# Performance work log

Measured on AMD Instinct MI355X. Metric: run time of the kernel, lower is better.

Reference implementation:

```python
import jax, jax.numpy as jnp
import numpy as np

N = 100000   # nodes
E = 1600000  # edges
G = 1000     # graphs
S = 32       # state_dim
H = 128      # hidden_dim_message / hidden_dim_output
F = 1        # num_features (edge coulomb)
ROUNDS = 5
NEG_SLOPE = 0.01
LN_EPS = 1e-5


def _ln(x, g, b):
    m = jnp.mean(x, axis=-1, keepdims=True)
    v = jnp.var(x, axis=-1, keepdims=True)
    return (x - m) / jnp.sqrt(v + LN_EPS) * g + b


def _lrelu(x):
    return jnp.where(x >= 0, x, NEG_SLOPE * x)


def _kaiming(k, shape):
    # torch kaiming_normal_(mode='fan_out', nonlinearity='leaky_relu'); W stored [in,out]
    gain = np.sqrt(2.0 / (1.0 + NEG_SLOPE ** 2))
    std = gain / np.sqrt(shape[1])
    return jax.random.normal(k, shape, dtype=jnp.float32) * std


def setup_inputs() -> dict:
    key = jax.random.key(0)
    ks = jax.random.split(key, 10)
    return {
        'node_from': jax.random.randint(ks[0], (E,), 0, N),
        'node_to': jax.random.randint(ks[1], (E,), 0, N),
        'edge_coulomb': jax.random.normal(ks[2], (E, F), dtype=jnp.float32),
        'node_graph_index': jax.random.randint(ks[3], (N,), 0, G),
        'num_nodes': N,
        'num_graphs': G,
        # message_net params
        'W1': _kaiming(ks[4], (S + F, H)), 'b1': jnp.zeros((H,), jnp.float32),
        'g1': jnp.ones((H,), jnp.float32), 'be1': jnp.zeros((H,), jnp.float32),
        'W2': _kaiming(ks[5], (H, S)), 'b2': jnp.zeros((S,), jnp.float32),
        'g2': jnp.ones((S,), jnp.float32), 'be2': jnp.zeros((S,), jnp.float32),
        # output_net params
        'Wo1': _kaiming(ks[6], (S, H)), 'bo1': jnp.zeros((H,), jnp.float32),
        'go': jnp.ones((H,), jnp.float32), 'beo': jnp.zeros((H,), jnp.float32),
        'Wo2': _kaiming(ks[7], (H, 2)), 'bo2': jnp.zeros((2,), jnp.float32),
    }


def reference(node_from, node_to, edge_coulomb, node_graph_index, num_nodes, num_graphs,
              W1, b1, g1, be1, W2, b2, g2, be2, Wo1, bo1, go, beo, Wo2, bo2):
    state = jnp.zeros((num_nodes, S), dtype=edge_coulomb.dtype)
    for _ in range(ROUNDS):
        inp = jnp.concatenate([state[node_from], edge_coulomb], axis=1)  # [E, S+F]
        h = _lrelu(_ln(inp @ W1 + b1, g1, be1))                           # [E, H]
        msg = _lrelu(_ln(h @ W2 + b2, g2, be2))                           # [E, S]
        state = state + jax.ops.segment_sum(msg, node_to, num_segments=num_nodes)
    graph_state = jax.ops.segment_sum(state, node_graph_index, num_segments=num_graphs)  # [G, S]
    h = _lrelu(_ln(graph_state @ Wo1 + bo1, go, beo))
    ev = h @ Wo2 + bo2                                                    # [G, 2]
    mu = ev[:, :1]
    var = jax.nn.softplus(ev[:, 1:])
    return jnp.concatenate([mu, var], axis=1)
```

## Files before the change

kernel.cpp:

```cpp
#include <hip/hip_runtime.h>
#include <hip/hip_bf16.h>

#define NN 100000
#define NE 1600000
#define NG 1000
#define SS 32
#define HH 128
#define ROUNDS 5

constexpr float NEG = 0.01f;
constexpr float EPS = 1e-5f;

constexpr long al4(long x)  { return (x + 3) & ~3L; }
constexpr long al16(long x) { return (x + 15) & ~15L; }

constexpr long OFF_STATE = 0;
constexpr long OFF_GS    = OFF_STATE + (long)NN * SS;
constexpr long OFF_W1T   = OFF_GS + (long)NG * SS;
constexpr long OFF_B1    = OFF_W1T + HH * 33;
constexpr long OFF_G1    = OFF_B1 + HH;
constexpr long OFF_BE1   = OFF_G1 + HH;
constexpr long OFF_W2    = OFF_BE1 + HH;
constexpr long OFF_B2    = OFF_W2 + HH * SS;
constexpr long OFF_G2    = OFF_B2 + SS;
constexpr long OFF_BE2   = OFF_G2 + SS;
constexpr long OFF_WO1   = OFF_BE2 + SS;
constexpr long OFF_BO1   = OFF_WO1 + SS * HH;
constexpr long OFF_GO    = OFF_BO1 + HH;
constexpr long OFF_BEO   = OFF_GO + HH;
constexpr long OFF_WO2   = OFF_BEO + HH;
constexpr long OFF_BO2   = OFF_WO2 + HH * 2;
constexpr long OFF_W1L   = al4(OFF_BO2 + 2);
constexpr long OFF_WSC   = OFF_W1L + HH;
constexpr long OFF_W1B   = al4(OFF_WSC + 2);
constexpr long OFF_W2F   = OFF_W1B + 2048;
constexpr long OFF_WPK   = OFF_W2F + 2048;
constexpr long OFF_Z0P   = OFF_WPK + 192;
constexpr long W_END     = OFF_Z0P + 68;
constexpr long OFF_DELTA = al4(W_END);
constexpr long F_Z      = al4(W_END);
constexpr long F_START  = al4(F_Z + (long)NN * 68);
constexpr long F_CURSOR = F_START + NN + 4;
constexpr long F_SSTART = F_CURSOR + NN;
constexpr long F_SCUR   = F_SSTART + NN + 4;
constexpr long F_BSUM   = F_SCUR + NN;
constexpr long F_GDEG   = F_BSUM + 512;
constexpr long F_GSTART = F_GDEG + NG;
constexpr long F_GCUR   = F_GSTART + NG + 4;
constexpr long F_GLIST  = F_GCUR + NG;
constexpr long F_EPK    = al16(F_GLIST + NN);
constexpr long F_SP     = F_EPK + (long)NE * 2;
constexpr long F_MSG    = al16(F_SP + NE);
constexpr long F_RC     = F_MSG;
constexpr long WS_TOTAL = F_MSG + (long)NE * 16;
constexpr long WS_FALLBACK = OFF_DELTA + (long)NN * SS;
constexpr int  NBLK_N  = (NN + 255) / 256;
constexpr int  CHSHIFT_E = 19;
constexpr int  NCH_E     = (NE + (1 << CHSHIFT_E) - 1) >> CHSHIFT_E;
constexpr int  CHSHIFT_P = 20;
constexpr int  NCH_P     = (NE + (1 << CHSHIFT_P) - 1) >> CHSHIFT_P;

typedef float f32x4 __attribute__((ext_vector_type(4)));
typedef unsigned int u32x4 __attribute__((ext_vector_type(4)));
typedef short s16x8 __attribute__((ext_vector_type(8)));

__device__ __forceinline__ s16x8 as_s16x8(u32x4 u) {
    union { u32x4 a; s16x8 b; } c; c.a = u; return c.b;
}
__device__ __forceinline__ float bf2f(unsigned short u) {
    union { unsigned int i; float f; } v;
    v.i = ((unsigned int)u) << 16;
    return v.f;
}
__device__ __forceinline__ float lo_bf(unsigned int p) {
    union { unsigned int i; float f; } v; v.i = p << 16; return v.f;
}
__device__ __forceinline__ float hi_bf(unsigned int p) {
    union { unsigned int i; float f; } v; v.i = p & 0xFFFF0000u; return v.f;
}
__device__ __forceinline__ unsigned short f2bf(float f) {
    union { float f; unsigned int u; } x; x.f = f;
    return (unsigned short)((x.u + 0x7FFFu + ((x.u >> 16) & 1u)) >> 16);
}
__device__ __forceinline__ unsigned int pack_bf2(float a, float b) {
    return (unsigned int)f2bf(a) | ((unsigned int)f2bf(b) << 16);
}
#if defined(__has_builtin)
#if __has_builtin(__builtin_amdgcn_cvt_pk_bf16_f32)
#define HAVE_CVT_PK_BF16 1
#endif
#endif
__device__ __forceinline__ unsigned int cvt2bf(float a, float b) {
#ifdef HAVE_CVT_PK_BF16
    auto r = __builtin_amdgcn_cvt_pk_bf16_f32(a, b);
    unsigned int u; __builtin_memcpy(&u, &r, 4); return u;
#else
    return pack_bf2(a, b);
#endif
}
template <int CTRL>
__device__ __forceinline__ float ror_add(float x) {
    int v = __builtin_amdgcn_update_dpp(0, __float_as_int(x), CTRL, 0xF, 0xF, true);
    return x + __int_as_float(v);
}
__device__ __forceinline__ float row_reduce16(float x) {
    x = ror_add<0x121>(x);
    x = ror_add<0x122>(x);
    x = ror_add<0x124>(x);
    x = ror_add<0x128>(x);
    return x;
}
__device__ __forceinline__ int is_bf16(const void* g1raw) {
    return (((const unsigned int*)g1raw)[0] & 0xFFFFu) != 0u;
}
__device__ __forceinline__ float ldf(const void* p, long idx, int bf) {
    return bf ? bf2f(((const unsigned short*)p)[idx]) : ((const float*)p)[idx];
}

__global__ void prep_kernel(
    const void* __restrict__ W1,  const void* __restrict__ b1,
    const void* __restrict__ g1,  const void* __restrict__ be1,
    const void* __restrict__ W2,  const void* __restrict__ b2,
    const void* __restrict__ g2,  const void* __restrict__ be2,
    const void* __restrict__ Wo1, const void* __restrict__ bo1,
    const void* __restrict__ go,  const void* __restrict__ beo,
    const void* __restrict__ Wo2, const void* __restrict__ bo2,
    float* __restrict__ ws)
{
    const int bf = is_bf16(g1);
    long idx = (long)blockIdx.x * blockDim.x + threadIdx.x;
    if (idx < (long)NN * SS) { ws[OFF_STATE + idx] = 0.f; ws[OFF_DELTA + idx] = 0.f; }
    if (idx < (long)NG * SS) ws[OFF_GS + idx] = 0.f;
    if (idx < NN) { ((int*)(ws + F_CURSOR))[idx] = 0; ((int*)(ws + F_SCUR))[idx] = 0; }
    if (idx < NG) ((int*)(ws + F_GDEG))[idx] = 0;
    if (idx < 33 * HH) {
        int i = (int)(idx / HH), k = (int)(idx % HH);
        ws[OFF_W1T + (long)k * 33 + i] = ldf(W1, idx, bf);
    }
    if (idx < HH) {
        ws[OFF_B1  + idx] = ldf(b1,  idx, bf);
        ws[OFF_G1  + idx] = ldf(g1,  idx, bf);
        ws[OFF_BE1 + idx] = ldf(be1, idx, bf);
        ws[OFF_BO1 + idx] = ldf(bo1, idx, bf);
        ws[OFF_GO  + idx] = ldf(go,  idx, bf);
        ws[OFF_BEO + idx] = ldf(beo, idx, bf);
        ws[OFF_W1L + idx] = ldf(W1, (long)32 * HH + idx, bf);
    }
    if (idx == 0) {
        float sw = 0.f, sq = 0.f;
        float sb = 0.f, qb = 0.f, db = 0.f;
        for (int i = 0; i < HH; i++) {
            float w = ldf(W1, (long)32 * HH + i, bf);
            float x = ldf(b1, i, bf);
            sw += w; sq = fmaf(w, w, sq);
            sb += x; qb = fmaf(x, x, qb); db = fmaf(x, w, db);
        }
        ws[OFF_WSC] = sw; ws[OFF_WSC + 1] = sq;
        float* z0s = ws + OFF_Z0P + 64;
        z0s[0] = sb; z0s[1] = qb; z0s[2] = db; z0s[3] = 0.f;
    }
    if (idx < 64) {
        ((unsigned int*)(ws + OFF_Z0P))[idx] =
            cvt2bf(ldf(b1, 2 * idx, bf), ldf(b1, 2 * idx + 1, bf));
    }
    if (idx < HH * SS) ws[OFF_W2 + idx] = ldf(W2, idx, bf);
    if (idx < SS) {
        ws[OFF_B2  + idx] = ldf(b2,  idx, bf);
        ws[OFF_G2  + idx] = ldf(g2,  idx, bf);
        ws[OFF_BE2 + idx] = ldf(be2, idx, bf);
    }
    if (idx < SS * HH) ws[OFF_WO1 + idx] = ldf(Wo1, idx, bf);
    if (idx < HH * 2)  ws[OFF_WO2 + idx] = ldf(Wo2, idx, bf);
    if (idx < 2)       ws[OFF_BO2 + idx] = ldf(bo2, idx, bf);
    if (idx < 2048) {
        int w = (int)idx;
        int qq = w & 3, L = (w >> 2) & 63, t = (int)(w >> 8);
        int k0 = (L >> 4) * 8 + 2 * qq;
        int n  = t * 16 + (L & 15);
        ((unsigned int*)(ws + OFF_W1B))[w] =
            pack_bf2(ldf(W1, (long)k0 * HH + n, bf), ldf(W1, (long)(k0 + 1) * HH + n, bf));
    }
    if (idx < 2048) {
        int w = (int)idx;
        int qq = w & 3, L = (w >> 2) & 63, t2 = (w >> 8) & 1, ks = (int)(w >> 9);
        int k0 = ks * 32 + (L >> 4) * 8 + 2 * qq;
        int n  = t2 * 16 + (L & 15);
        float v0 = ldf(W2, (long)k0 * SS + n, bf);
        float v1 = ldf(W2, (long)(k0 + 1) * SS + n, bf);
        ((unsigned int*)(ws + OFF_W2F))[w] = pack_bf2(v0, v1);
    }
    if (idx < 192) {
        int w = (int)idx;
        int grp = w / 12, rem = w % 12, slot = rem >> 2, q = rem & 3;
        int ks = grp >> 2, quad = grp & 3;
        int n = ks * 32 + quad * 8 + 2 * q;
        float v0, v1;
        if (slot == 0)      { v0 = ldf(W1, (long)32 * HH + n, bf); v1 = ldf(W1, (long)32 * HH + n + 1, bf); }
        else if (slot == 1) { v0 = ldf(g1, n, bf);  v1 = ldf(g1, n + 1, bf); }
        else                { v0 = ldf(be1, n, bf); v1 = ldf(be1, n + 1, bf); }
        ((unsigned int*)(ws + OFF_WPK))[w] = pack_bf2(v0, v1);
    }
}

__global__ void fillseq_kernel(const int* __restrict__ nfrom, const int* __restrict__ nto,
                               float* ws) {
    int e = blockIdx.x * 256 + threadIdx.x;
    if (e < NE) {
        int u = nfrom[e];
        int v = nto[e];
        int drank = atomicAdd(&((int*)(ws + F_CURSOR))[v], 1);
        int srank = atomicAdd(&((int*)(ws + F_SCUR))[u], 1);
        uint2 o; o.x = (unsigned int)drank; o.y = (unsigned int)srank;
        *(uint2*)((unsigned int*)(ws + F_RC) + (long)e * 2) = o;
    }
}

__global__ void scan1_kernel(float* ws, long degOff, long startOff) {
    __shared__ int sh[256];
    int* deg   = (int*)(ws + degOff);
    int* start = (int*)(ws + startOff);
    int* bsum  = (int*)(ws + F_BSUM);
    int i = blockIdx.x * 256 + threadIdx.x;
    int x = (i < NN) ? deg[i] : 0;
    sh[threadIdx.x] = x;
    __syncthreads();
    for (int off = 1; off < 256; off <<= 1) {
        int t = (threadIdx.x >= off) ? sh[threadIdx.x - off] : 0;
        __syncthreads();
        sh[threadIdx.x] += t;
        __syncthreads();
    }
    int incl = sh[threadIdx.x];
    if (i < NN) start[i] = incl - x;
    if (threadIdx.x == 255) bsum[blockIdx.x] = incl;
}

__global__ void scan2p_kernel(float* ws) {
    __shared__ int sh[512];
    int* bsum = (int*)(ws + F_BSUM);
    int t = threadIdx.x;
    int x = (t < NBLK_N) ? bsum[t] : 0;
    sh[t] = x;
    __syncthreads();
    for (int off = 1; off < 512; off <<= 1) {
        int v = (t >= off) ? sh[t - off] : 0;
        __syncthreads();
        sh[t] += v;
        __syncthreads();
    }
    if (t < NBLK_N) bsum[t] = sh[t] - x;
}

__global__ void scan3_kernel(float* ws, long startOff) {
    int* start  = (int*)(ws + startOff);
    int* bsum   = (int*)(ws + F_BSUM);
    int i = blockIdx.x * 256 + threadIdx.x;
    if (i < NN) {
        start[i] += bsum[i >> 8];
        if (i == 0) start[NN] = NE;
    }
}

__global__ void epkc_kernel(const int* __restrict__ nfrom, const void* __restrict__ ec,
                            const void* __restrict__ g1raw, float* ws, int chunk) {
    int e = blockIdx.x * 256 + threadIdx.x;
    if (e < NE) {
        uint2 rc = *(const uint2*)((const unsigned int*)(ws + F_RC) + (long)e * 2);
        int u = nfrom[e];
        int spos = ((const int*)(ws + F_SSTART))[u] + (int)rc.y;
        if ((spos >> CHSHIFT_E) == chunk) {
            union { float f; unsigned int i; } c; c.f = ldf(ec, e, is_bf16(g1raw));
            uint2 o; o.x = (unsigned int)u; o.y = c.i;
            *(uint2*)((unsigned int*)(ws + F_EPK) + (long)spos * 2) = o;
        }
    }
}

__global__ void spc_kernel(const int* __restrict__ nfrom, const int* __restrict__ nto,
                           float* ws, int chunk) {
    int e = blockIdx.x * 256 + threadIdx.x;
    if (e < NE) {
        uint2 rc = *(const uint2*)((const unsigned int*)(ws + F_RC) + (long)e * 2);
        int dpos = ((const int*)(ws + F_START))[nto[e]] + (int)rc.x;
        if ((dpos >> CHSHIFT_P) == chunk) {
            int spos = ((const int*)(ws + F_SSTART))[nfrom[e]] + (int)rc.y;
            ((int*)(ws + F_SP))[dpos] = spos;
        }
    }
}

__global__ void ghist_kernel(const int* __restrict__ gidx, float* ws) {
    int i = blockIdx.x * 256 + threadIdx.x;
    if (i < NN) atomicAdd(&((int*)(ws + F_GDEG))[gidx[i]], 1);
}

__global__ void gscan_kernel(float* ws) {
    __shared__ int sh[1024];
    int* deg   = (int*)(ws + F_GDEG);
    int* start = (int*)(ws + F_GSTART);
    int* cur   = (int*)(ws + F_GCUR);
    int t = threadIdx.x;
    int x = (t < NG) ? deg[t] : 0;
    sh[t] = x;
    __syncthreads();
    for (int off = 1; off < 1024; off <<= 1) {
        int v = (t >= off) ? sh[t - off] : 0;
        __syncthreads();
        sh[t] += v;
        __syncthreads();
    }
    if (t < NG) { start[t] = sh[t] - x; cur[t] = sh[t] - x; }
    if (t == 0) start[NG] = NN;
}

__global__ void gfill_kernel(const int* __restrict__ gidx, float* ws) {
    int i = blockIdx.x * 256 + threadIdx.x;
    if (i < NN) {
        int pos = atomicAdd(&((int*)(ws + F_GCUR))[gidx[i]], 1);
        ((int*)(ws + F_GLIST))[pos] = i;
    }
}

__launch_bounds__(256)
__global__ void node_kernel(float* __restrict__ ws, const u32x4* __restrict__ mb, int do_z)
{
    __shared__ unsigned short zl[4][16 * 136];
    __shared__ float stl[64 * 33];
    const long nbase = (long)blockIdx.x * 64;

    {
        int t = threadIdx.x;
        int vl = t >> 2, sub = t & 3;
        long v = nbase + vl;
        if (v < NN) {
            const int* start = (const int*)(ws + F_START);
            const int* SPp   = (const int*)(ws + F_SP);
            int s0 = start[v], s1 = start[v + 1];
            float* st = ws + OFF_STATE + v * SS + sub * 8;
            float a0 = st[0], a1 = st[1], a2 = st[2], a3 = st[3];
            float a4 = st[4], a5 = st[5], a6 = st[6], a7 = st[7];
            int p = s0;
            for (; p + 7 < s1; p += 8) {
                int q0 = SPp[p],     q1 = SPp[p + 1], q2 = SPp[p + 2], q3 = SPp[p + 3];
                int q4 = SPp[p + 4], q5 = SPp[p + 5], q6 = SPp[p + 6], q7 = SPp[p + 7];
                u32x4 m0 = mb[(long)q0 * 4 + sub];
                u32x4 m1 = mb[(long)q1 * 4 + sub];
                u32x4 m2 = mb[(long)q2 * 4 + sub];
                u32x4 m3 = mb[(long)q3 * 4 + sub];
                u32x4 m4 = mb[(long)q4 * 4 + sub];
                u32x4 m5 = mb[(long)q5 * 4 + sub];
                u32x4 m6 = mb[(long)q6 * 4 + sub];
                u32x4 m7 = mb[(long)q7 * 4 + sub];
                a0 += lo_bf(m0[0]); a1 += hi_bf(m0[0]);
                a2 += lo_bf(m0[1]); a3 += hi_bf(m0[1]);
                a4 += lo_bf(m0[2]); a5 += hi_bf(m0[2]);
                a6 += lo_bf(m0[3]); a7 += hi_bf(m0[3]);
                a0 += lo_bf(m1[0]); a1 += hi_bf(m1[0]);
                a2 += lo_bf(m1[1]); a3 += hi_bf(m1[1]);
                a4 += lo_bf(m1[2]); a5 += hi_bf(m1[2]);
                a6 += lo_bf(m1[3]); a7 += hi_bf(m1[3]);
                a0 += lo_bf(m2[0]); a1 += hi_bf(m2[0]);
                a2 += lo_bf(m2[1]); a3 += hi_bf(m2[1]);
                a4 += lo_bf(m2[2]); a5 += hi_bf(m2[2]);
                a6 += lo_bf(m2[3]); a7 += hi_bf(m2[3]);
                a0 += lo_bf(m3[0]); a1 += hi_bf(m3[0]);
                a2 += lo_bf(m3[1]); a3 += hi_bf(m3[1]);
                a4 += lo_bf(m3[2]); a5 += hi_bf(m3[2]);
                a6 += lo_bf(m3[3]); a7 += hi_bf(m3[3]);
                a0 += lo_bf(m4[0]); a1 += hi_bf(m4[0]);
                a2 += lo_bf(m4[1]); a3 += hi_bf(m4[1]);
                a4 += lo_bf(m4[2]); a5 += hi_bf(m4[2]);
                a6 += lo_bf(m4[3]); a7 += hi_bf(m4[3]);
                a0 += lo_bf(m5[0]); a1 += hi_bf(m5[0]);
                a2 += lo_bf(m5[1]); a3 += hi_bf(m5[1]);
                a4 += lo_bf(m5[2]); a5 += hi_bf(m5[2]);
                a6 += lo_bf(m5[3]); a7 += hi_bf(m5[3]);
                a0 += lo_bf(m6[0]); a1 += hi_bf(m6[0]);
                a2 += lo_bf(m6[1]); a3 += hi_bf(m6[1]);
                a4 += lo_bf(m6[2]); a5 += hi_bf(m6[2]);
                a6 += lo_bf(m6[3]); a7 += hi_bf(m6[3]);
                a0 += lo_bf(m7[0]); a1 += hi_bf(m7[0]);
                a2 += lo_bf(m7[1]); a3 += hi_bf(m7[1]);
                a4 += lo_bf(m7[2]); a5 += hi_bf(m7[2]);
                a6 += lo_bf(m7[3]); a7 += hi_bf(m7[3]);
            }
            for (; p + 3 < s1; p += 4) {
                int q0 = SPp[p], q1 = SPp[p + 1], q2 = SPp[p + 2], q3 = SPp[p + 3];
                u32x4 m0 = mb[(long)q0 * 4 + sub];
                u32x4 m1 = mb[(long)q1 * 4 + sub];
                u32x4 m2 = mb[(long)q2 * 4 + sub];
                u32x4 m3 = mb[(long)q3 * 4 + sub];
                a0 += lo_bf(m0[0]); a1 += hi_bf(m0[0]);
                a2 += lo_bf(m0[1]); a3 += hi_bf(m0[1]);
                a4 += lo_bf(m0[2]); a5 += hi_bf(m0[2]);
                a6 += lo_bf(m0[3]); a7 += hi_bf(m0[3]);
                a0 += lo_bf(m1[0]); a1 += hi_bf(m1[0]);
                a2 += lo_bf(m1[1]); a3 += hi_bf(m1[1]);
                a4 += lo_bf(m1[2]); a5 += hi_bf(m1[2]);
                a6 += lo_bf(m1[3]); a7 += hi_bf(m1[3]);
                a0 += lo_bf(m2[0]); a1 += hi_bf(m2[0]);
                a2 += lo_bf(m2[1]); a3 += hi_bf(m2[1]);
                a4 += lo_bf(m2[2]); a5 += hi_bf(m2[2]);
                a6 += lo_bf(m2[3]); a7 += hi_bf(m2[3]);
                a0 += lo_bf(m3[0]); a1 += hi_bf(m3[0]);
                a2 += lo_bf(m3[1]); a3 += hi_bf(m3[1]);
                a4 += lo_bf(m3[2]); a5 += hi_bf(m3[2]);
                a6 += lo_bf(m3[3]); a7 += hi_bf(m3[3]);
            }
            for (; p < s1; ++p) {
                int spv = SPp[p];
                u32x4 m = mb[(long)spv * 4 + sub];
                a0 += lo_bf(m[0]); a1 += hi_bf(m[0]);
                a2 += lo_bf(m[1]); a3 += hi_bf(m[1]);
                a4 += lo_bf(m[2]); a5 += hi_bf(m[2]);
                a6 += lo_bf(m[3]); a7 += hi_bf(m[3]);
            }
            st[0] = a0; st[1] = a1; st[2] = a2; st[3] = a3;
            st[4] = a4; st[5] = a5; st[6] = a6; st[7] = a7;
            float* sl = stl + vl * 33 + sub * 8;
            sl[0] = a0; sl[1] = a1; sl[2] = a2; sl[3] = a3;
            sl[4] = a4; sl[5] = a5; sl[6] = a6; sl[7] = a7;
        }
    }
    if (!do_z) return;
    __syncthreads();

    const int wv = threadIdx.x >> 6, lane = threadIdx.x & 63;
    const int col = lane & 15, quad = lane >> 4;
    const long vbase = nbase + wv * 16;
    if (vbase >= NN) return;

    const float* sl = stl + (wv * 16 + col) * 33 + quad * 8;
    float st[8];
#pragma unroll
    for (int j = 0; j < 8; j++) st[j] = sl[j];

    u32x4 au;
    au[0] = cvt2bf(st[0], st[1]);
    au[1] = cvt2bf(st[2], st[3]);
    au[2] = cvt2bf(st[4], st[5]);
    au[3] = cvt2bf(st[6], st[7]);
    s16x8 af = as_s16x8(au);

    const u32x4* W1B = (const u32x4*)(ws + OFF_W1B);
    const float* B1 = ws + OFF_B1;
    f32x4 acc[8];
#pragma unroll
    for (int t = 0; t < 8; t++) {
        float bb = B1[t * 16 + col];
        acc[t][0] = bb; acc[t][1] = bb; acc[t][2] = bb; acc[t][3] = bb;
        acc[t] = __builtin_amdgcn_mfma_f32_16x16x32_bf16(af, as_s16x8(W1B[t * 64 + lane]), acc[t], 0, 0, 0);
    }

    float s[4] = {0.f, 0.f, 0.f, 0.f}, q[4] = {0.f, 0.f, 0.f, 0.f}, d[4] = {0.f, 0.f, 0.f, 0.f};
    const float* W1L = ws + OFF_W1L;
#pragma unroll
    for (int t = 0; t < 8; t++) {
        float wl = W1L[t * 16 + col];
#pragma unroll
        for (int r = 0; r < 4; r++) {
            float z = acc[t][r];
            s[r] += z; q[r] = fmaf(z, z, q[r]); d[r] = fmaf(z, wl, d[r]);
        }
    }
#pragma unroll
    for (int r = 0; r < 4; r++) {
        float sr = row_reduce16(s[r]);
        float qr = row_reduce16(q[r]);
        float dr = row_reduce16(d[r]);
        if (col == 0) {
            f32x4 o; o[0] = sr; o[1] = qr; o[2] = dr; o[3] = 0.f;
            *(f32x4*)(ws + F_Z + (vbase + quad * 4 + r) * 68 + 64) = o;
        }
    }

    unsigned short* zw_ = zl[wv];
#pragma unroll
    for (int t = 0; t < 8; t++) {
        unsigned int p01 = cvt2bf(acc[t][0], acc[t][1]);
        unsigned int p23 = cvt2bf(acc[t][2], acc[t][3]);
        unsigned short* b = zw_ + quad * (4 * 136) + t * 16 + col;
        b[0]       = (unsigned short)p01;
        b[136]     = (unsigned short)(p01 >> 16);
        b[2 * 136] = (unsigned short)p23;
        b[3 * 136] = (unsigned short)(p23 >> 16);
    }
    unsigned int* zg = (unsigned int*)(ws + F_Z);
#pragma unroll
    for (int it = 0; it < 4; it++) {
        int byte = it * 1024 + lane * 16;
        int node = byte >> 8;
        int ko   = (byte & 255) >> 2;
        u32x4 val = *(const u32x4*)(zw_ + node * 136 + ((byte & 255) >> 1));
        *(u32x4*)(zg + (vbase + node) * 68L + ko) = val;
    }
}

template <int R0>
__launch_bounds__(256)
__global__ void edge_src_kernel(const float* __restrict__ ws, uint2* __restrict__ msgout)
{
    const int lane = threadIdx.x & 63, wv = threadIdx.x >> 6;
    const int col = lane & 15, quad = lane >> 4;

    const u32x4* W2Fp = (const u32x4*)(ws + OFF_W2F);
    u32x4 w2f[8];
#pragma unroll
    for (int i = 0; i < 8; i++) w2f[i] = W2Fp[i * 64 + lane];
    u32x4 wlp[4], gp[4], bep[4];
    const u32x4* WPKp = (const u32x4*)(ws + OFF_WPK);
#pragma unroll
    for (int ks = 0; ks < 4; ks++) {
        const u32x4* W = WPKp + (ks * 4 + quad) * 3;
        wlp[ks] = W[0]; gp[ks] = W[1]; bep[ks] = W[2];
    }
    f32x4 g2h[2], be2h[2], b2h[2];
#pragma unroll
    for (int t2 = 0; t2 < 2; t2++) {
        g2h[t2]  = *(const f32x4*)(ws + OFF_G2  + t2 * 16 + quad * 4);
        be2h[t2] = *(const f32x4*)(ws + OFF_BE2 + t2 * 16 + quad * 4);
        b2h[t2]  = *(const f32x4*)(ws + OFF_B2  + t2 * 16 + quad * 4);
    }
    const float sw1 = ws[OFF_WSC], sqw1 = ws[OFF_WSC + 1];

    f32x4 zst0;
    u32x4 zw0[4];
    if (R0) {
        zst0 = *(const f32x4*)(ws + OFF_Z0P + 64);
#pragma unroll
        for (int ks = 0; ks < 4; ks++)
            zw0[ks] = *(const u32x4*)((const unsigned int*)(ws + OFF_Z0P) + ks * 16 + quad * 4);
    }

    const uint2* EPKp = (const uint2*)((const unsigned int*)(ws + F_EPK));
    const unsigned int* Zp = (const unsigned int*)(ws + F_Z);
    const long tbase = ((long)blockIdx.x * 4 + wv) * 4;

    uint2 epk[4];
#pragma unroll
    for (int k = 0; k < 4; k++)
        epk[k] = EPKp[(tbase + k) * 16 + col];
    f32x4 zst[4];
    u32x4 zwc[4];
    if (!R0) {
#pragma unroll
        for (int k = 0; k < 4; k++)
            zst[k] = *(const f32x4*)(ws + F_Z + (long)(int)epk[k].x * 68 + 64);
        const unsigned int* zrow0 = Zp + (long)(int)epk[0].x * 68;
#pragma unroll
        for (int ks = 0; ks < 4; ks++)
            zwc[ks] = *(const u32x4*)(zrow0 + ks * 16 + quad * 4);
    }

#pragma unroll
    for (int k = 0; k < 4; k++) {
        const int epos = (int)((tbase + k) * 16) + col;
        union { unsigned int i; float f; } cc; cc.i = epk[k].y;
        const float ecv = cc.f;

        u32x4 zwn[4];
        if (!R0 && k < 3) {
            const unsigned int* zrown = Zp + (long)(int)epk[k + 1].x * 68;
#pragma unroll
            for (int ks = 0; ks < 4; ks++)
                zwn[ks] = *(const u32x4*)(zrown + ks * 16 + quad * 4);
        }

        f32x4 zs = R0 ? zst0 : zst[k];
        float sumh = fmaf(ecv, sw1, zs[0]);
        float sqh  = fmaf(ecv, fmaf(ecv, sqw1, 2.f * zs[2]), zs[1]);
        float mean = sumh * (1.f / HH);
        float var  = fmaxf(sqh * (1.f / HH) - mean * mean, 0.f);
        float inv  = rsqrtf(var + EPS);
        const float alpha = inv, beta = -mean * inv;

        f32x4 acc2[2];
        acc2[0] = b2h[0]; acc2[1] = b2h[1];

#pragma unroll
        for (int ks = 0; ks < 4; ks++) {
            u32x4 zwv = R0 ? zw0[ks] : zwc[ks];
            u32x4 hu;
#pragma unroll
            for (int w = 0; w < 4; w++) {
                float z0 = lo_bf(zwv[w]), z1 = hi_bf(zwv[w]);
                float h0 = fmaf(ecv, lo_bf(wlp[ks][w]), z0);
                float h1 = fmaf(ecv, hi_bf(wlp[ks][w]), z1);
                h0 = fmaf(h0, alpha, beta);
                h1 = fmaf(h1, alpha, beta);
                h0 = fmaf(h0, lo_bf(gp[ks][w]), lo_bf(bep[ks][w]));
                h1 = fmaf(h1, hi_bf(gp[ks][w]), hi_bf(bep[ks][w]));
                h0 = fmaxf(h0, NEG * h0);
                h1 = fmaxf(h1, NEG * h1);
                hu[w] = cvt2bf(h0, h1);
            }
            s16x8 hf = as_s16x8(hu);
            acc2[0] = __builtin_amdgcn_mfma_f32_16x16x32_bf16(as_s16x8(w2f[ks * 2 + 0]), hf, acc2[0], 0, 0, 0);
            acc2[1] = __builtin_amdgcn_mfma_f32_16x16x32_bf16(as_s16x8(w2f[ks * 2 + 1]), hf, acc2[1], 0, 0, 0);
        }

        float s2 = 0.f, q2 = 0.f;
#pragma unroll
        for (int t2 = 0; t2 < 2; t2++)
#pragma unroll
            for (int r = 0; r < 4; r++) { float vv = acc2[t2][r]; s2 += vv; q2 = fmaf(vv, vv, q2); }
        s2 += __shfl_xor(s2, 16); q2 += __shfl_xor(q2, 16);
        s2 += __shfl_xor(s2, 32); q2 += __shfl_xor(q2, 32);
        float mean2 = s2 * (1.f / SS);
        float var2  = fmaxf(q2 * (1.f / SS) - mean2 * mean2, 0.f);
        float inv2  = rsqrtf(var2 + EPS);
        const float a2 = inv2, b2c = -mean2 * inv2;

        uint2* dst = msgout + (long)epos * 8;
#pragma unroll
        for (int t2 = 0; t2 < 2; t2++) {
            float m0 = fmaf(fmaf(acc2[t2][0], a2, b2c), g2h[t2][0], be2h[t2][0]);
            float m1 = fmaf(fmaf(acc2[t2][1], a2, b2c), g2h[t2][1], be2h[t2][1]);
            float m2 = fmaf(fmaf(acc2[t2][2], a2, b2c), g2h[t2][2], be2h[t2][2]);
            float m3 = fmaf(fmaf(acc2[t2][3], a2, b2c), g2h[t2][3], be2h[t2][3]);
            m0 = fmaxf(m0, NEG * m0); m1 = fmaxf(m1, NEG * m1);
            m2 = fmaxf(m2, NEG * m2); m3 = fmaxf(m3, NEG * m3);
            uint2 o; o.x = cvt2bf(m0, m1); o.y = cvt2bf(m2, m3);
            dst[t2 * 4 + quad] = o;
        }

        if (!R0 && k < 3) {
#pragma unroll
            for (int ks = 0; ks < 4; ks++) zwc[ks] = zwn[ks];
        }
    }
}

__launch_bounds__(256)
__global__ void graph_gather_kernel(float* __restrict__ ws)
{
    int t = blockIdx.x * 256 + threadIdx.x;
    int g = t >> 5;
    if (g >= NG) return;
    int j = t & 31;
    const int* start = (const int*)(ws + F_GSTART);
    const int* list  = (const int*)(ws + F_GLIST);
    int s0 = start[g], s1 = start[g + 1];
    float acc = 0.f;
    for (int p = s0; p < s1; ++p)
        acc += ws[OFF_STATE + (long)list[p] * SS + j];
    ws[OFF_GS + (long)g * SS + j] = acc;
}

__launch_bounds__(256)
__global__ void edge_atomic_kernel(const int* __restrict__ nfrom, const int* __restrict__ nto,
                                   const void* __restrict__ ec, const void* __restrict__ g1raw,
                                   const float* __restrict__ cws, float* delta)
{
    int e = blockIdx.x * 256 + threadIdx.x;
    if (e >= NE) return;
    const float* state = cws + OFF_STATE;
    const float* W1T = cws + OFF_W1T;
    const float* B1  = cws + OFF_B1;
    const float* G1  = cws + OFF_G1;
    const float* BE1 = cws + OFF_BE1;
    const float* W2  = cws + OFF_W2;
    const float* B2  = cws + OFF_B2;
    const float* G2  = cws + OFF_G2;
    const float* BE2 = cws + OFF_BE2;
    int u = nfrom[e];
    float inp[33];
    const float4* srow = (const float4*)(state + (long)u * SS);
#pragma unroll
    for (int i = 0; i < 8; i++) {
        float4 v = srow[i];
        inp[i * 4 + 0] = v.x; inp[i * 4 + 1] = v.y;
        inp[i * 4 + 2] = v.z; inp[i * 4 + 3] = v.w;
    }
    inp[32] = ldf(ec, e, is_bf16(g1raw));
    float sum = 0.f, sq = 0.f;
    for (int k = 0; k < HH; k++) {
        const float* wr = W1T + k * 33;
        float a = B1[k];
#pragma unroll
        for (int i = 0; i < 33; i++) a = fmaf(inp[i], wr[i], a);
        sum += a; sq = fmaf(a, a, sq);
    }
    float mean = sum * (1.f / HH);
    float var  = sq * (1.f / HH) - mean * mean;
    float inv  = rsqrtf(var + EPS);
    float msg[SS];
#pragma unroll
    for (int j = 0; j < SS; j++) msg[j] = B2[j];
    for (int k = 0; k < HH; k++) {
        const float* wr = W1T + k * 33;
        float a = B1[k];
#pragma unroll
        for (int i = 0; i < 33; i++) a = fmaf(inp[i], wr[i], a);
        float hk = fmaf((a - mean) * inv, G1[k], BE1[k]);
        hk = hk >= 0.f ? hk : NEG * hk;
        const float* w2r = W2 + k * SS;
#pragma unroll
        for (int j = 0; j < SS; j++) msg[j] = fmaf(hk, w2r[j], msg[j]);
    }
    float s2 = 0.f, q2 = 0.f;
#pragma unroll
    for (int j = 0; j < SS; j++) { s2 += msg[j]; q2 = fmaf(msg[j], msg[j], q2); }
    float m2 = s2 * (1.f / SS);
    float v2 = q2 * (1.f / SS) - m2 * m2;
    float i2 = rsqrtf(v2 + EPS);
    int v = nto[e];
    float* drow = delta + (long)v * SS;
#pragma unroll
    for (int j = 0; j < SS; j++) {
        float mj = fmaf((msg[j] - m2) * i2, G2[j], BE2[j]);
        mj = mj >= 0.f ? mj : NEG * mj;
        atomicAdd(drow + j, mj);
    }
}

__global__ void update_kernel(float* ws)
{
    long idx = (long)blockIdx.x * blockDim.x + threadIdx.x;
    if (idx < (long)NN * SS) {
        ws[OFF_STATE + idx] += ws[OFF_DELTA + idx];
        ws[OFF_DELTA + idx] = 0.f;
    }
}

__global__ void graph_kernel(const int* __restrict__ gidx, float* ws)
{
    long idx = (long)blockIdx.x * blockDim.x + threadIdx.x;
    if (idx < (long)NN * SS) {
        int i = (int)(idx >> 5);
        int j = (int)(idx & 31);
        atomicAdd(&ws[OFF_GS + (long)gidx[i] * SS + j], ws[OFF_STATE + idx]);
    }
}

__global__ void readout_kernel(const float* __restrict__ ws, const void* __restrict__ g1raw,
                               void* __restrict__ out)
{
    int g = blockIdx.x;
    int j = threadIdx.x;
    __shared__ float row[SS];
    __shared__ float buf[HH];
    __shared__ float p0[HH];
    __shared__ float p1[HH];

    const float* gs  = ws + OFF_GS;
    const float* Wo1 = ws + OFF_WO1;
    if (j < SS) row[j] = gs[(long)g * SS + j];
    __syncthreads();

    float a = ws[OFF_BO1 + j];
#pragma unroll
    for (int i = 0; i < SS; i++) a = fmaf(row[i], Wo1[i * HH + j], a);
    buf[j] = a;
    __syncthreads();

    float sum = 0.f, sq = 0.f;
    for (int i = 0; i < HH; i++) { float x = buf[i]; sum += x; sq = fmaf(x, x, sq); }
    float mean = sum * (1.f / HH);
    float var  = sq * (1.f / HH) - mean * mean;
    float inv  = rsqrtf(var + EPS);
    float h = fmaf((a - mean) * inv, ws[OFF_GO + j], ws[OFF_BEO + j]);
    h = h >= 0.f ? h : NEG * h;

    p0[j] = h * ws[OFF_WO2 + j * 2 + 0];
    p1[j] = h * ws[OFF_WO2 + j * 2 + 1];
    __syncthreads();

    if (j == 0) {
        float e0 = ws[OFF_BO2 + 0], e1 = ws[OFF_BO2 + 1];
        for (int i = 0; i < HH; i++) { e0 += p0[i]; e1 += p1[i]; }
        float sp = (e1 > 20.f) ? e1 : log1pf(expf(e1));
        if (is_bf16(g1raw)) {
            __hip_bfloat16* o = (__hip_bfloat16*)out;
            o[g * 2 + 0] = __float2bfloat16(e0);
            o[g * 2 + 1] = __float2bfloat16(sp);
        } else {
            float* o = (float*)out;
            o[g * 2 + 0] = e0;
            o[g * 2 + 1] = sp;
        }
    }
}

extern "C" void kernel_launch(void* const* d_in, const int* in_sizes, int n_in,
                              void* d_out, int out_size, void* d_ws, size_t ws_size,
                              hipStream_t stream)
{
    const int* nfrom = (const int*)d_in[0];
    const int* nto   = (const int*)d_in[1];
    const void* ec   = d_in[2];
    const int* gidx  = (const int*)d_in[3];
    const void* W1  = d_in[6];
    const void* b1  = d_in[7];
    const void* g1  = d_in[8];
    const void* be1 = d_in[9];
    const void* W2  = d_in[10];
    const void* b2  = d_in[11];
    const void* g2  = d_in[12];
    const void* be2 = d_in[13];
    const void* Wo1 = d_in[14];
    const void* bo1 = d_in[15];
    const void* go  = d_in[16];
    const void* beo = d_in[17];
    const void* Wo2 = d_in[18];
    const void* bo2 = d_in[19];

    float* ws = (float*)d_ws;
    if (ws_size < (size_t)WS_FALLBACK * sizeof(float)) return;
    const bool gather = ws_size >= (size_t)WS_TOTAL * sizeof(float);

    const int nsBlocks = (int)(((long)NN * SS + 255) / 256);
    const int eBlocks  = (NE + 255) / 256;
    const int efBlocks = NE / 256;
    const int ndBlocks = (NN + 63) / 64;
    const int nBlocks1 = (NN + 255) / 256;

    prep_kernel<<<nsBlocks, 256, 0, stream>>>(W1, b1, g1, be1, W2, b2, g2, be2,
                                              Wo1, bo1, go, beo, Wo2, bo2, ws);
    if (gather) {
        uint2* msgp = (uint2*)(ws + F_MSG);
        const u32x4* mbp = (const u32x4*)(ws + F_MSG);
        fillseq_kernel<<<eBlocks, 256, 0, stream>>>(nfrom, nto, ws);
        scan1_kernel<<<NBLK_N, 256, 0, stream>>>(ws, F_CURSOR, F_START);
        scan2p_kernel<<<1, 512, 0, stream>>>(ws);
        scan3_kernel<<<NBLK_N, 256, 0, stream>>>(ws, F_START);
        scan1_kernel<<<NBLK_N, 256, 0, stream>>>(ws, F_SCUR, F_SSTART);
        scan2p_kernel<<<1, 512, 0, stream>>>(ws);
        scan3_kernel<<<NBLK_N, 256, 0, stream>>>(ws, F_SSTART);
        for (int c = 0; c < NCH_E; c++)
            epkc_kernel<<<eBlocks, 256, 0, stream>>>(nfrom, ec, g1, ws, c);
        for (int c = 0; c < NCH_P; c++)
            spc_kernel<<<eBlocks, 256, 0, stream>>>(nfrom, nto, ws, c);
        ghist_kernel<<<nBlocks1, 256, 0, stream>>>(gidx, ws);
        gscan_kernel<<<1, 1024, 0, stream>>>(ws);
        gfill_kernel<<<nBlocks1, 256, 0, stream>>>(gidx, ws);
        for (int r = 0; r < ROUNDS; r++) {
            if (r == 0) edge_src_kernel<1><<<efBlocks, 256, 0, stream>>>(ws, msgp);
            else        edge_src_kernel<0><<<efBlocks, 256, 0, stream>>>(ws, msgp);
            node_kernel<<<ndBlocks, 256, 0, stream>>>(ws, mbp, (r < ROUNDS - 1) ? 1 : 0);
        }
        graph_gather_kernel<<<(NG * 32 + 255) / 256, 256, 0, stream>>>(ws);
    } else {
        for (int r = 0; r < ROUNDS; r++) {
            edge_atomic_kernel<<<eBlocks, 256, 0, stream>>>(nfrom, nto, ec, g1, ws, ws + OFF_DELTA);
            update_kernel<<<nsBlocks, 256, 0, stream>>>(ws);
        }
        graph_kernel<<<nsBlocks, 256, 0, stream>>>(gidx, ws);
    }
    readout_kernel<<<NG, HH, 0, stream>>>(ws, g1, (void*)d_out);
}
```

Measured before the change: 1.062 ms.

## Merge CSR conversion passes, pad Z rows, double edges per wave, skip unused zeroing

Fuses the chunked epkc and spc conversion loops into one chunked conv kernel that computes both source and destination positions per edge, cutting redundant passes over the edge arrays. Pads the per-node Z rows from 68 to 80 floats and aligns them to 16, so gathered row reads are better aligned. The edge kernel now processes two groups of 4 tiles per wave, halving the grid. The delta buffer is only zeroed on the fallback path, and LDS state stores are skipped when Z is not needed. Padding Z costs more workspace, and the wider per-wave loop reduces the number of waves available to hide gather latency.

```diff
diff --git a/kernel.cpp b/kernel.cpp
--- a/kernel.cpp
+++ b/kernel.cpp
@@ -13,6 +13,8 @@
 
 constexpr long al4(long x)  { return (x + 3) & ~3L; }
 constexpr long al16(long x) { return (x + 15) & ~15L; }
+
+constexpr int ZSTR = 80;
 
 constexpr long OFF_STATE = 0;
 constexpr long OFF_GS    = OFF_STATE + (long)NN * SS;
@@ -38,8 +40,8 @@
 constexpr long OFF_Z0P   = OFF_WPK + 192;
 constexpr long W_END     = OFF_Z0P + 68;
 constexpr long OFF_DELTA = al4(W_END);
-constexpr long F_Z      = al4(W_END);
-constexpr long F_START  = al4(F_Z + (long)NN * 68);
+constexpr long F_Z      = al16(W_END);
+constexpr long F_START  = al4(F_Z + (long)NN * ZSTR);
 constexpr long F_CURSOR = F_START + NN + 4;
 constexpr long F_SSTART = F_CURSOR + NN;
 constexpr long F_SCUR   = F_SSTART + NN + 4;
@@ -55,10 +57,8 @@
 constexpr long WS_TOTAL = F_MSG + (long)NE * 16;
 constexpr long WS_FALLBACK = OFF_DELTA + (long)NN * SS;
 constexpr int  NBLK_N  = (NN + 255) / 256;
-constexpr int  CHSHIFT_E = 19;
-constexpr int  NCH_E     = (NE + (1 << CHSHIFT_E) - 1) >> CHSHIFT_E;
-constexpr int  CHSHIFT_P = 20;
-constexpr int  NCH_P     = (NE + (1 << CHSHIFT_P) - 1) >> CHSHIFT_P;
+constexpr int  CHSHIFT_C = 19;
+constexpr int  NCH_C     = (NE + (1 << CHSHIFT_C) - 1) >> CHSHIFT_C;
 
 typedef float f32x4 __attribute__((ext_vector_type(4)));
 typedef unsigned int u32x4 __attribute__((ext_vector_type(4)));
@@ -125,11 +125,14 @@
     const void* __restrict__ Wo1, const void* __restrict__ bo1,
     const void* __restrict__ go,  const void* __restrict__ beo,
     const void* __restrict__ Wo2, const void* __restrict__ bo2,
-    float* __restrict__ ws)
+    float* __restrict__ ws, int zeroDelta)
 {
     const int bf = is_bf16(g1);
     long idx = (long)blockIdx.x * blockDim.x + threadIdx.x;
-    if (idx < (long)NN * SS) { ws[OFF_STATE + idx] = 0.f; ws[OFF_DELTA + idx] = 0.f; }
+    if (idx < (long)NN * SS) {
+        ws[OFF_STATE + idx] = 0.f;
+        if (zeroDelta) ws[OFF_DELTA + idx] = 0.f;
+    }
     if (idx < (long)NG * SS) ws[OFF_GS + idx] = 0.f;
     if (idx < NN) { ((int*)(ws + F_CURSOR))[idx] = 0; ((int*)(ws + F_SCUR))[idx] = 0; }
     if (idx < NG) ((int*)(ws + F_GDEG))[idx] = 0;
@@ -261,29 +264,22 @@
     }
 }
 
-__global__ void epkc_kernel(const int* __restrict__ nfrom, const void* __restrict__ ec,
-                            const void* __restrict__ g1raw, float* ws, int chunk) {
+__global__ void conv_kernel(const int* __restrict__ nfrom, const int* __restrict__ nto,
+                            const void* __restrict__ ec, const void* __restrict__ g1raw,
+                            float* ws, int chunk) {
     int e = blockIdx.x * 256 + threadIdx.x;
     if (e < NE) {
         uint2 rc = *(const uint2*)((const unsigned int*)(ws + F_RC) + (long)e * 2);
         int u = nfrom[e];
+        int v = nto[e];
         int spos = ((const int*)(ws + F_SSTART))[u] + (int)rc.y;
-        if ((spos >> CHSHIFT_E) == chunk) {
+        int dpos = ((const int*)(ws + F_START))[v] + (int)rc.x;
+        if ((spos >> CHSHIFT_C) == chunk) {
             union { float f; unsigned int i; } c; c.f = ldf(ec, e, is_bf16(g1raw));
             uint2 o; o.x = (unsigned int)u; o.y = c.i;
             *(uint2*)((unsigned int*)(ws + F_EPK) + (long)spos * 2) = o;
         }
-    }
-}
-
-__global__ void spc_kernel(const int* __restrict__ nfrom, const int* __restrict__ nto,
-                           float* ws, int chunk) {
-    int e = blockIdx.x * 256 + threadIdx.x;
-    if (e < NE) {
-        uint2 rc = *(const uint2*)((const unsigned int*)(ws + F_RC) + (long)e * 2);
-        int dpos = ((const int*)(ws + F_START))[nto[e]] + (int)rc.x;
-        if ((dpos >> CHSHIFT_P) == chunk) {
-            int spos = ((const int*)(ws + F_SSTART))[nfrom[e]] + (int)rc.y;
+        if ((dpos >> CHSHIFT_C) == chunk) {
             ((int*)(ws + F_SP))[dpos] = spos;
         }
     }
@@ -417,9 +413,11 @@
             }
             st[0] = a0; st[1] = a1; st[2] = a2; st[3] = a3;
             st[4] = a4; st[5] = a5; st[6] = a6; st[7] = a7;
-            float* sl = stl + vl * 33 + sub * 8;
-            sl[0] = a0; sl[1] = a1; sl[2] = a2; sl[3] = a3;
-            sl[4] = a4; sl[5] = a5; sl[6] = a6; sl[7] = a7;
+            if (do_z) {
+                float* sl = stl + vl * 33 + sub * 8;
+                sl[0] = a0; sl[1] = a1; sl[2] = a2; sl[3] = a3;
+                sl[4] = a4; sl[5] = a5; sl[6] = a6; sl[7] = a7;
+            }
         }
     }
     if (!do_z) return;
@@ -470,7 +468,7 @@
         float dr = row_reduce16(d[r]);
         if (col == 0) {
             f32x4 o; o[0] = sr; o[1] = qr; o[2] = dr; o[3] = 0.f;
-            *(f32x4*)(ws + F_Z + (vbase + quad * 4 + r) * 68 + 64) = o;
+            *(f32x4*)(ws + F_Z + (vbase + quad * 4 + r) * (long)ZSTR + 64) = o;
         }
     }
 
@@ -492,7 +490,7 @@
         int node = byte >> 8;
         int ko   = (byte & 255) >> 2;
         u32x4 val = *(const u32x4*)(zw_ + node * 136 + ((byte & 255) >> 1));
-        *(u32x4*)(zg + (vbase + node) * 68L + ko) = val;
+        *(u32x4*)(zg + (vbase + node) * (long)ZSTR + ko) = val;
     }
 }
 
@@ -534,99 +532,103 @@
 
     const uint2* EPKp = (const uint2*)((const unsigned int*)(ws + F_EPK));
     const unsigned int* Zp = (const unsigned int*)(ws + F_Z);
-    const long tbase = ((long)blockIdx.x * 4 + wv) * 4;
-
-    uint2 epk[4];
-#pragma unroll
-    for (int k = 0; k < 4; k++)
-        epk[k] = EPKp[(tbase + k) * 16 + col];
-    f32x4 zst[4];
-    u32x4 zwc[4];
-    if (!R0) {
+    const long wavebase = ((long)blockIdx.x * 4 + wv) * 8;
+
+    for (int g = 0; g < 2; g++) {
+        const long tbase = wavebase + g * 4;
+
+        uint2 epk[4];
 #pragma unroll
         for (int k = 0; k < 4; k++)
-            zst[k] = *(const f32x4*)(ws + F_Z + (long)(int)epk[k].x * 68 + 64);
-        const unsigned int* zrow0 = Zp + (long)(int)epk[0].x * 68;
-#pragma unroll
-        for (int ks = 0; ks < 4; ks++)
-            zwc[ks] = *(const u32x4*)(zrow0 + ks * 16 + quad * 4);
-    }
-
-#pragma unroll
-    for (int k = 0; k < 4; k++) {
-        const int epos = (int)((tbase + k) * 16) + col;
-        union { unsigned int i; float f; } cc; cc.i = epk[k].y;
-        const float ecv = cc.f;
-
-        u32x4 zwn[4];
-        if (!R0 && k < 3) {
-            const unsigned int* zrown = Zp + (long)(int)epk[k + 1].x * 68;
+            epk[k] = EPKp[(tbase + k) * 16 + col];
+        f32x4 zst[4];
+        u32x4 zwc[4];
+        if (!R0) {
+#pragma unroll
+            for (int k = 0; k < 4; k++)
+                zst[k] = *(const f32x4*)(ws + F_Z + (long)(int)epk[k].x * ZSTR + 64);
+            const unsigned int* zrow0 = Zp + (long)(int)epk[0].x * ZSTR;
 #pragma unroll
             for (int ks = 0; ks < 4; ks++)
-                zwn[ks] = *(const u32x4*)(zrown + ks * 16 + quad * 4);
-        }
-
-        f32x4 zs = R0 ? zst0 : zst[k];
-        float sumh = fmaf(ecv, sw1, zs[0]);
-        float sqh  = fmaf(ecv, fmaf(ecv, sqw1, 2.f * zs[2]), zs[1]);
-        float mean = sumh * (1.f / HH);
-        float var  = fmaxf(sqh * (1.f / HH) - mean * mean, 0.f);
-        float inv  = rsqrtf(var + EPS);
-        const float alpha = inv, beta = -mean * inv;
-
-        f32x4 acc2[2];
-        acc2[0] = b2h[0]; acc2[1] = b2h[1];
-
-#pragma unroll
-        for (int ks = 0; ks < 4; ks++) {
-            u32x4 zwv = R0 ? zw0[ks] : zwc[ks];
-            u32x4 hu;
-#pragma unroll
-            for (int w = 0; w < 4; w++) {
-                float z0 = lo_bf(zwv[w]), z1 = hi_bf(zwv[w]);
-                float h0 = fmaf(ecv, lo_bf(wlp[ks][w]), z0);
-                float h1 = fmaf(ecv, hi_bf(wlp[ks][w]), z1);
-                h0 = fmaf(h0, alpha, beta);
-                h1 = fmaf(h1, alpha, beta);
-                h0 = fmaf(h0, lo_bf(gp[ks][w]), lo_bf(bep[ks][w]));
-                h1 = fmaf(h1, hi_bf(gp[ks][w]), hi_bf(bep[ks][w]));
-                h0 = fmaxf(h0, NEG * h0);
-                h1 = fmaxf(h1, NEG * h1);
-                hu[w] = cvt2bf(h0, h1);
+                zwc[ks] = *(const u32x4*)(zrow0 + ks * 16 + quad * 4);
+        }
+
+#pragma unroll
+        for (int k = 0; k < 4; k++) {
+            const int epos = (int)((tbase + k) * 16) + col;
+            union { unsigned int i; float f; } cc; cc.i = epk[k].y;
+            const float ecv = cc.f;
+
+            u32x4 zwn[4];
+            if (!R0 && k < 3) {
+                const unsigned int* zrown = Zp + (long)(int)epk[k + 1].x * ZSTR;
+#pragma unroll
+                for (int ks = 0; ks < 4; ks++)
+                    zwn[ks] = *(const u32x4*)(zrown + ks * 16 + quad * 4);
             }
-            s16x8 hf = as_s16x8(hu);
-            acc2[0] = __builtin_amdgcn_mfma_f32_16x16x32_bf16(as_s16x8(w2f[ks * 2 + 0]), hf, acc2[0], 0, 0, 0);
-            acc2[1] = __builtin_amdgcn_mfma_f32_16x16x32_bf16(as_s16x8(w2f[ks * 2 + 1]), hf, acc2[1], 0, 0, 0);
-        }
-
-        float s2 = 0.f, q2 = 0.f;
-#pragma unroll
-        for (int t2 = 0; t2 < 2; t2++)
-#pragma unroll
-            for (int r = 0; r < 4; r++) { float vv = acc2[t2][r]; s2 += vv; q2 = fmaf(vv, vv, q2); }
-        s2 += __shfl_xor(s2, 16); q2 += __shfl_xor(q2, 16);
-        s2 += __shfl_xor(s2, 32); q2 += __shfl_xor(q2, 32);
-        float mean2 = s2 * (1.f / SS);
-        float var2  = fmaxf(q2 * (1.f / SS) - mean2 * mean2, 0.f);
-        float inv2  = rsqrtf(var2 + EPS);
-        const float a2 = inv2, b2c = -mean2 * inv2;
-
-        uint2* dst = msgout + (long)epos * 8;
-#pragma unroll
-        for (int t2 = 0; t2 < 2; t2++) {
-            float m0 = fmaf(fmaf(acc2[t2][0], a2, b2c), g2h[t2][0], be2h[t2][0]);
-            float m1 = fmaf(fmaf(acc2[t2][1], a2, b2c), g2h[t2][1], be2h[t2][1]);
-            float m2 = fmaf(fmaf(acc2[t2][2], a2, b2c), g2h[t2][2], be2h[t2][2]);
-            float m3 = fmaf(fmaf(acc2[t2][3], a2, b2c), g2h[t2][3], be2h[t2][3]);
-            m0 = fmaxf(m0, NEG * m0); m1 = fmaxf(m1, NEG * m1);
-            m2 = fmaxf(m2, NEG * m2); m3 = fmaxf(m3, NEG * m3);
-            uint2 o; o.x = cvt2bf(m0, m1); o.y = cvt2bf(m2, m3);
-            dst[t2 * 4 + quad] = o;
-        }
-
-        if (!R0 && k < 3) {
-#pragma unroll
-            for (int ks = 0; ks < 4; ks++) zwc[ks] = zwn[ks];
+
+            f32x4 zs = R0 ? zst0 : zst[k];
+            float sumh = fmaf(ecv, sw1, zs[0]);
+            float sqh  = fmaf(ecv, fmaf(ecv, sqw1, 2.f * zs[2]), zs[1]);
+            float mean = sumh * (1.f / HH);
+            float var  = fmaxf(sqh * (1.f / HH) - mean * mean, 0.f);
+            float inv  = rsqrtf(var + EPS);
+            const float alpha = inv, beta = -mean * inv;
+
+            f32x4 acc2[2];
+            acc2[0] = b2h[0]; acc2[1] = b2h[1];
+
+#pragma unroll
+            for (int ks = 0; ks < 4; ks++) {
+                u32x4 zwv = R0 ? zw0[ks] : zwc[ks];
+                u32x4 hu;
+#pragma unroll
+                for (int w = 0; w < 4; w++) {
+                    float z0 = lo_bf(zwv[w]), z1 = hi_bf(zwv[w]);
+                    float h0 = fmaf(ecv, lo_bf(wlp[ks][w]), z0);
+                    float h1 = fmaf(ecv, hi_bf(wlp[ks][w]), z1);
+                    h0 = fmaf(h0, alpha, beta);
+                    h1 = fmaf(h1, alpha, beta);
+                    h0 = fmaf(h0, lo_bf(gp[ks][w]), lo_bf(bep[ks][w]));
+                    h1 = fmaf(h1, hi_bf(gp[ks][w]), hi_bf(bep[ks][w]));
+                    h0 = fmaxf(h0, NEG * h0);
+                    h1 = fmaxf(h1, NEG * h1);
+                    hu[w] = cvt2bf(h0, h1);
+                }
+                s16x8 hf = as_s16x8(hu);
+                acc2[0] = __builtin_amdgcn_mfma_f32_16x16x32_bf16(as_s16x8(w2f[ks * 2 + 0]), hf, acc2[0], 0, 0, 0);
+                acc2[1] = __builtin_amdgcn_mfma_f32_16x16x32_bf16(as_s16x8(w2f[ks * 2 + 1]), hf, acc2[1], 0, 0, 0);
+            }
+
+            float s2 = 0.f, q2 = 0.f;
+#pragma unroll
+            for (int t2 = 0; t2 < 2; t2++)
+#pragma unroll
+                for (int r = 0; r < 4; r++) { float vv = acc2[t2][r]; s2 += vv; q2 = fmaf(vv, vv, q2); }
+            s2 += __shfl_xor(s2, 16); q2 += __shfl_xor(q2, 16);
+            s2 += __shfl_xor(s2, 32); q2 += __shfl_xor(q2, 32);
+            float mean2 = s2 * (1.f / SS);
+            float var2  = fmaxf(q2 * (1.f / SS) - mean2 * mean2, 0.f);
+            float inv2  = rsqrtf(var2 + EPS);
+            const float a2 = inv2, b2c = -mean2 * inv2;
+
+            uint2* dst = msgout + (long)epos * 8;
+#pragma unroll
+            for (int t2 = 0; t2 < 2; t2++) {
+                float m0 = fmaf(fmaf(acc2[t2][0], a2, b2c), g2h[t2][0], be2h[t2][0]);
+                float m1 = fmaf(fmaf(acc2[t2][1], a2, b2c), g2h[t2][1], be2h[t2][1]);
+                float m2 = fmaf(fmaf(acc2[t2][2], a2, b2c), g2h[t2][2], be2h[t2][2]);
+                float m3 = fmaf(fmaf(acc2[t2][3], a2, b2c), g2h[t2][3], be2h[t2][3]);
+                m0 = fmaxf(m0, NEG * m0); m1 = fmaxf(m1, NEG * m1);
+                m2 = fmaxf(m2, NEG * m2); m3 = fmaxf(m3, NEG * m3);
+                uint2 o; o.x = cvt2bf(m0, m1); o.y = cvt2bf(m2, m3);
+                dst[t2 * 4 + quad] = o;
+            }
+
+            if (!R0 && k < 3) {
+#pragma unroll
+                for (int ks = 0; ks < 4; ks++) zwc[ks] = zwn[ks];
+            }
         }
     }
 }
@@ -811,12 +813,13 @@
 
     const int nsBlocks = (int)(((long)NN * SS + 255) / 256);
     const int eBlocks  = (NE + 255) / 256;
-    const int efBlocks = NE / 256;
+    const int efBlocks = NE / 512;
     const int ndBlocks = (NN + 63) / 64;
     const int nBlocks1 = (NN + 255) / 256;
 
     prep_kernel<<<nsBlocks, 256, 0, stream>>>(W1, b1, g1, be1, W2, b2, g2, be2,
-                                              Wo1, bo1, go, beo, Wo2, bo2, ws);
+                                              Wo1, bo1, go, beo, Wo2, bo2, ws,
+                                              gather ? 0 : 1);
     if (gather) {
         uint2* msgp = (uint2*)(ws + F_MSG);
         const u32x4* mbp = (const u32x4*)(ws + F_MSG);
@@ -827,10 +830,8 @@
         scan1_kernel<<<NBLK_N, 256, 0, stream>>>(ws, F_SCUR, F_SSTART);
         scan2p_kernel<<<1, 512, 0, stream>>>(ws);
         scan3_kernel<<<NBLK_N, 256, 0, stream>>>(ws, F_SSTART);
-        for (int c = 0; c < NCH_E; c++)
-            epkc_kernel<<<eBlocks, 256, 0, stream>>>(nfrom, ec, g1, ws, c);
-        for (int c = 0; c < NCH_P; c++)
-            spc_kernel<<<eBlocks, 256, 0, stream>>>(nfrom, nto, ws, c);
+        for (int c = 0; c < NCH_C; c++)
+            conv_kernel<<<eBlocks, 256, 0, stream>>>(nfrom, nto, ec, g1, ws, c);
         ghist_kernel<<<nBlocks1, 256, 0, stream>>>(gidx, ws);
         gscan_kernel<<<1, 1024, 0, stream>>>(ws);
         gfill_kernel<<<nBlocks1, 256, 0, stream>>>(gidx, ws);
```

After: 1.430 ms. +34.6%, slower.
